# Optimization experiments

Hardware: AMD Instinct MI355X
Metric: run time of the kernel (lower is better)

Reference implementation:

```python
import jax, jax.numpy as jnp
import numpy as np

B, N_MODES, N_CLASSES = 200000, 64, 10
HBAR = 2.0


def setup_inputs() -> dict:
    key = jax.random.key(0)
    k1, k2, k3, k4 = jax.random.split(key, 4)
    twoN = 2 * N_MODES
    x = jax.random.normal(k1, (B, N_MODES), dtype=jnp.float32)
    # Ansatz (learned Gaussian channel): symplectic-like matrix S and displacement d.
    S = jax.random.normal(k2, (twoN, twoN), dtype=jnp.float32) * (1.0 / np.sqrt(twoN))
    d = jax.random.normal(k3, (twoN,), dtype=jnp.float32)
    bias = jnp.zeros((N_MODES,), dtype=jnp.float32)
    W = jax.random.normal(k4, (N_CLASSES, N_MODES), dtype=jnp.float32) * (1.0 / np.sqrt(N_MODES))
    b = jnp.zeros((N_CLASSES,), dtype=jnp.float32)
    return {"x": x, "S": S, "d": d, "bias": bias, "W": W, "b": b}


def reference(x, S, d, bias, W, b):
    # Vacuum mean vector is zero; displacing mode i by alpha = x_i/sqrt(2*hbar)
    # shifts the x-quadrature (even indices, xpxp ordering) by sqrt(2*hbar)*Re(alpha) = x_i.
    Bn = x.shape[0]
    twoN = 2 * x.shape[1]
    mu = jnp.zeros((Bn, twoN), dtype=x.dtype).at[:, ::2].set(x)  # [B, 2N]
    # Ansatz: affine symplectic map mu' = S mu + d (cov transform S cov S^T does
    # not affect the expectation-value homodyne readout mu_x).
    mu_out = mu @ S.T + d  # [B, 2N]
    # Homodyne x-quadrature readout per mode + bias.
    readout = mu_out[:, ::2] + bias  # [B, N]
    return readout @ W.T + b  # [B, n_classes]
```

## Files before the change

### kernel.cpp

```cpp
#include <hip/hip_runtime.h>

#define NM 64
#define NC 10

__global__ __launch_bounds__(640) void cv2d_precompute(
    const float* __restrict__ S,
    const float* __restrict__ d,
    const float* __restrict__ bias,
    const float* __restrict__ W,
    const float* __restrict__ bvec,
    float* __restrict__ ws)
{
    const int t = threadIdx.x;
    const int twoN = 2 * NM;
    if (t < NM * NC) {
        const int m = t / NC;
        const int c = t - m * NC;
        float acc = 0.f;
        #pragma unroll
        for (int k = 0; k < NM; ++k) {
            acc += S[(2 * k) * twoN + 2 * m] * W[c * NM + k];
        }
        ws[m * NC + c] = acc;
    }
    if (t < NC) {
        float acc = bvec[t];
        #pragma unroll
        for (int k = 0; k < NM; ++k) {
            acc += (d[2 * k] + bias[k]) * W[t * NM + k];
        }
        ws[NM * NC + t] = acc;
    }
}

__global__ __launch_bounds__(256) void cv2d_main(
    const float* __restrict__ x,
    const float* __restrict__ Mc,
    float* __restrict__ out,
    int Bn)
{
    const int row = blockIdx.x * 256 + threadIdx.x;
    if (row >= Bn) return;

    const float4* __restrict__ xr = (const float4*)(x + (size_t)row * NM);

    float acc[NC];
    #pragma unroll
    for (int c = 0; c < NC; ++c) acc[c] = Mc[NM * NC + c];

    #pragma unroll
    for (int q = 0; q < NM / 4; ++q) {
        const float4 v = xr[q];
        #pragma unroll
        for (int c = 0; c < NC; ++c) {
            acc[c] += v.x * Mc[(4 * q + 0) * NC + c];
            acc[c] += v.y * Mc[(4 * q + 1) * NC + c];
            acc[c] += v.z * Mc[(4 * q + 2) * NC + c];
            acc[c] += v.w * Mc[(4 * q + 3) * NC + c];
        }
    }

    float2* __restrict__ o = (float2*)(out + (size_t)row * NC);
    #pragma unroll
    for (int c = 0; c < NC; c += 2) {
        o[c / 2] = make_float2(acc[c], acc[c + 1]);
    }
}

extern "C" void kernel_launch(void* const* d_in, const int* in_sizes, int n_in,
                              void* d_out, int out_size, void* d_ws, size_t ws_size,
                              hipStream_t stream) {
    const float* x    = (const float*)d_in[0];
    const float* S    = (const float*)d_in[1];
    const float* d    = (const float*)d_in[2];
    const float* bias = (const float*)d_in[3];
    const float* W    = (const float*)d_in[4];
    const float* bvec = (const float*)d_in[5];
    float* out = (float*)d_out;
    float* ws  = (float*)d_ws;

    const int Bn = in_sizes[0] / NM;

    cv2d_precompute<<<1, 640, 0, stream>>>(S, d, bias, W, bvec, ws);

    const int grid = (Bn + 255) / 256;
    cv2d_main<<<grid, 256, 0, stream>>>(x, ws, out, Bn);
}
```

Measured before the change: 106.5 us.

## Stage x rows through XOR-swizzled shared memory for coalesced loads

The main kernel now loads a 128-row tile of x cooperatively with consecutive threads reading consecutive float4s, which makes the global loads coalesced. The tile goes into shared memory with an XOR swizzle to avoid bank conflicts, and then each thread computes its own row from LDS. Previously each thread strided through its own 256-byte row. The precompute kernel is also split across 5 blocks of 128 threads. The cost is an extra LDS round trip and a barrier per block.

```diff
diff --git a/kernel.cpp b/kernel.cpp
--- a/kernel.cpp
+++ b/kernel.cpp
@@ -2,8 +2,10 @@
 
 #define NM 64
 #define NC 10
+#define BLOCK 128
+#define ROWS 128
 
-__global__ __launch_bounds__(640) void cv2d_precompute(
+__global__ __launch_bounds__(128) void cv2d_precompute(
     const float* __restrict__ S,
     const float* __restrict__ d,
     const float* __restrict__ bias,
@@ -11,7 +13,7 @@
     const float* __restrict__ bvec,
     float* __restrict__ ws)
 {
-    const int t = threadIdx.x;
+    const int t = blockIdx.x * 128 + threadIdx.x;
     const int twoN = 2 * NM;
     if (t < NM * NC) {
         const int m = t / NC;
@@ -33,37 +35,54 @@
     }
 }
 
-__global__ __launch_bounds__(256) void cv2d_main(
+__global__ __launch_bounds__(BLOCK) void cv2d_main(
     const float* __restrict__ x,
     const float* __restrict__ Mc,
     float* __restrict__ out,
     int Bn)
 {
-    const int row = blockIdx.x * 256 + threadIdx.x;
-    if (row >= Bn) return;
+    __shared__ float4 tile[ROWS * (NM / 4)];
 
-    const float4* __restrict__ xr = (const float4*)(x + (size_t)row * NM);
+    const int t = threadIdx.x;
+    const int base = blockIdx.x * ROWS;
+    const int rows = min(ROWS, Bn - base);
+    const int nf4 = rows * (NM / 4);
 
-    float acc[NC];
-    #pragma unroll
-    for (int c = 0; c < NC; ++c) acc[c] = Mc[NM * NC + c];
+    const float4* __restrict__ xg = (const float4*)(x + (size_t)base * NM);
 
     #pragma unroll
-    for (int q = 0; q < NM / 4; ++q) {
-        const float4 v = xr[q];
-        #pragma unroll
-        for (int c = 0; c < NC; ++c) {
-            acc[c] += v.x * Mc[(4 * q + 0) * NC + c];
-            acc[c] += v.y * Mc[(4 * q + 1) * NC + c];
-            acc[c] += v.z * Mc[(4 * q + 2) * NC + c];
-            acc[c] += v.w * Mc[(4 * q + 3) * NC + c];
+    for (int i = 0; i < (ROWS * NM / 4) / BLOCK; ++i) {
+        const int idx = i * BLOCK + t;
+        if (idx < nf4) {
+            const int r = idx >> 4;
+            const int q = idx & 15;
+            tile[(r << 4) | (q ^ (r & 7))] = xg[idx];
         }
     }
+    __syncthreads();
 
-    float2* __restrict__ o = (float2*)(out + (size_t)row * NC);
-    #pragma unroll
-    for (int c = 0; c < NC; c += 2) {
-        o[c / 2] = make_float2(acc[c], acc[c + 1]);
+    if (t < rows) {
+        float acc[NC];
+        #pragma unroll
+        for (int c = 0; c < NC; ++c) acc[c] = Mc[NM * NC + c];
+
+        #pragma unroll
+        for (int q = 0; q < NM / 4; ++q) {
+            const float4 v = tile[(t << 4) | (q ^ (t & 7))];
+            #pragma unroll
+            for (int c = 0; c < NC; ++c) {
+                acc[c] += v.x * Mc[(4 * q + 0) * NC + c];
+                acc[c] += v.y * Mc[(4 * q + 1) * NC + c];
+                acc[c] += v.z * Mc[(4 * q + 2) * NC + c];
+                acc[c] += v.w * Mc[(4 * q + 3) * NC + c];
+            }
+        }
+
+        float2* __restrict__ o = (float2*)(out + (size_t)(base + t) * NC);
+        #pragma unroll
+        for (int c = 0; c < NC; c += 2) {
+            o[c / 2] = make_float2(acc[c], acc[c + 1]);
+        }
     }
 }
 
@@ -81,8 +100,8 @@
 
     const int Bn = in_sizes[0] / NM;
 
-    cv2d_precompute<<<1, 640, 0, stream>>>(S, d, bias, W, bvec, ws);
+    cv2d_precompute<<<5, 128, 0, stream>>>(S, d, bias, W, bvec, ws);
 
-    const int grid = (Bn + 255) / 256;
-    cv2d_main<<<grid, 256, 0, stream>>>(x, ws, out, Bn);
+    const int grid = (Bn + ROWS - 1) / ROWS;
+    cv2d_main<<<grid, BLOCK, 0, stream>>>(x, ws, out, Bn);
 }
```

After: 106.3 us. Within noise of the previous version (-0.2%).
